# Kernel tuning notes

Measured on AMD Instinct MI355X. Metric: run time of the kernel, lower is better.

## Reference

```python
import jax, jax.numpy as jnp
import numpy as np

D = 512      # d_model
H = 8        # num_heads
DH = D // H  # d_head = 64
WIN = 10     # window_size
DFF = 2048   # d_ff
EPS = 1e-5   # LayerNorm eps


def _layernorm(x, w, b):
    mu = jnp.mean(x, axis=-1, keepdims=True)
    var = jnp.mean(jnp.square(x - mu), axis=-1, keepdims=True)
    return (x - mu) * jax.lax.rsqrt(var + EPS) * w + b


def setup_inputs() -> dict:
    key = jax.random.key(0)
    ks = jax.random.split(key, 8)
    s = 0.02
    inp = {
        "z": jax.random.normal(ks[0], (4, 2048, D), jnp.float32),
        "Wq": jax.random.normal(ks[1], (D, D), jnp.float32) * s,
        "bq": jnp.zeros((D,), jnp.float32),
        "Wk": jax.random.normal(ks[2], (D, D), jnp.float32) * s,
        "bk": jnp.zeros((D,), jnp.float32),
        "Wv": jax.random.normal(ks[3], (D, D), jnp.float32) * s,
        "bv": jnp.zeros((D,), jnp.float32),
        "Wo": jax.random.normal(ks[4], (D, D), jnp.float32) * s,
        "bo": jnp.zeros((D,), jnp.float32),
        "ln1_w": jnp.ones((D,), jnp.float32),
        "ln1_b": jnp.zeros((D,), jnp.float32),
        "W1": jax.random.normal(ks[5], (D, DFF), jnp.float32) * s,
        "b1": jnp.zeros((DFF,), jnp.float32),
        "W2": jax.random.normal(ks[6], (DFF, D), jnp.float32) * s,
        "b2": jnp.zeros((D,), jnp.float32),
        "ln2_w": jnp.ones((D,), jnp.float32),
        "ln2_b": jnp.zeros((D,), jnp.float32),
    }
    return inp


def reference(z, Wq, bq, Wk, bk, Wv, bv, Wo, bo, ln1_w, ln1_b, W1, b1, W2, b2, ln2_w, ln2_b):
    B, T, Dm = z.shape
    # projections -> [B, H, T, DH]
    q = (z @ Wq + bq).reshape(B, T, H, DH).transpose(0, 2, 1, 3)
    k = (z @ Wk + bk).reshape(B, T, H, DH).transpose(0, 2, 1, 3)
    v = (z @ Wv + bv).reshape(B, T, H, DH).transpose(0, 2, 1, 3)
    scale = 1.0 / jnp.sqrt(jnp.asarray(DH, z.dtype))
    scores = jnp.einsum('bhqd,bhkd->bhqk', q, k) * scale  # [B,H,T,T]
    idx = jnp.arange(T)
    dist = idx[:, None] - idx[None, :]
    valid = (dist >= 0) & (dist < WIN)
    neg = jnp.finfo(scores.dtype).min
    scores = jnp.where(valid[None, None], scores, neg)
    attn = jax.nn.softmax(scores, axis=-1)  # dropout is identity in eval
    out = jnp.einsum('bhqk,bhkd->bhqd', attn, v)
    out = out.transpose(0, 2, 1, 3).reshape(B, T, Dm)
    out = out @ Wo + bo
    z = _layernorm(z + out, ln1_w, ln1_b)
    # FFN with exact (erf) GELU, matching torch nn.GELU default
    ff = jax.nn.gelu(z @ W1 + b1, approximate=False) @ W2 + b2
    z = _layernorm(z + ff, ln2_w, ln2_b)
    return z
```

## Files before the change

### kernel.cpp

```cpp
#include <hip/hip_runtime.h>
#include <cstdint>
#include <cstddef>

#define DEV __device__ __forceinline__

typedef __bf16 bf16x8 __attribute__((ext_vector_type(8)));
typedef float f32x4 __attribute__((ext_vector_type(4)));
typedef unsigned short us8 __attribute__((ext_vector_type(8)));
typedef unsigned short us4 __attribute__((ext_vector_type(4)));

typedef const __attribute__((address_space(1))) unsigned int GUI;
typedef __attribute__((address_space(3))) unsigned int LUI;

DEV unsigned short f2bf(float f) {
  unsigned int u = __builtin_bit_cast(unsigned int, f);
  u += 0x7fffu + ((u >> 16) & 1u);
  return (unsigned short)(u >> 16);
}
DEV float bf2f(unsigned short h) {
  unsigned int u = ((unsigned int)h) << 16;
  return __builtin_bit_cast(float, u);
}

DEV void tr32(const float* __restrict__ in, unsigned short* __restrict__ out,
              int K, int N, int k0, int n0) {
  __shared__ float tile[32][33];
  const int tx = threadIdx.x & 31, ty = threadIdx.x >> 5;
#pragma unroll
  for (int i = 0; i < 32; i += 8)
    tile[ty + i][tx] = in[(size_t)(k0 + ty + i) * N + n0 + tx];
  __syncthreads();
#pragma unroll
  for (int i = 0; i < 32; i += 8)
    out[(size_t)(n0 + ty + i) * K + k0 + tx] = f2bf(tile[tx][ty + i]);
}

__global__ __launch_bounds__(256) void k_prep(
    const float* __restrict__ z, unsigned short* __restrict__ zb,
    const float* __restrict__ Wq, const float* __restrict__ Wk,
    const float* __restrict__ Wv, const float* __restrict__ Wo,
    unsigned short* __restrict__ Wsq,
    const float* __restrict__ W1, unsigned short* __restrict__ W1T,
    const float* __restrict__ W2, unsigned short* __restrict__ W2T,
    const float* __restrict__ bq, const float* __restrict__ bk,
    const float* __restrict__ bv, float* __restrict__ biasqkv) {
  const int j = blockIdx.x;
  const int tid = threadIdx.x;
  if (j < 4096) {
    int i = j * 256 + tid;
    float4 v = ((const float4*)z)[i];
    us4 o;
    o.x = f2bf(v.x); o.y = f2bf(v.y); o.z = f2bf(v.z); o.w = f2bf(v.w);
    *(us4*)(zb + (size_t)i * 4) = o;
  } else if (j < 5120) {
    int t = j - 4096;
    int mat = t >> 8, tile = t & 255;
    const float* in = mat == 0 ? Wq : mat == 1 ? Wk : mat == 2 ? Wv : Wo;
    tr32(in, Wsq + (size_t)mat * 262144, 512, 512, (tile >> 4) * 32, (tile & 15) * 32);
  } else if (j < 6144) {
    int t = j - 5120;
    tr32(W1, W1T, 512, 2048, (t / 64) * 32, (t % 64) * 32);
  } else if (j < 7168) {
    int t = j - 6144;
    tr32(W2, W2T, 2048, 512, (t / 16) * 32, (t % 16) * 32);
  } else {
    for (int i = tid; i < 1536; i += 256)
      biasqkv[i] = (i < 512) ? bq[i] : (i < 1024 ? bk[i - 512] : bv[i - 1024]);
  }
}

template <int MODE, int SPLITK>
DEV void gemm_body(const unsigned short* __restrict__ A,
                   const unsigned short* __restrict__ BT,
                   const float* __restrict__ bias,
                   unsigned short* __restrict__ outp,
                   int K, int N) {
  __shared__ __align__(16) unsigned short As[2 * 16384];
  __shared__ __align__(16) unsigned short Bs[2 * 16384];
  const int tid = threadIdx.x;
  const int wave = tid >> 6, lane = tid & 63;
  const int wm = wave >> 2, wn = wave & 3;

  const int nx = gridDim.x, ny = gridDim.y;
  const int nwg = nx * ny * SPLITK;
  const int lid = (blockIdx.z * ny + blockIdx.y) * nx + blockIdx.x;
  const int q8 = nwg >> 3, r8 = nwg & 7;
  const int xcd = lid & 7, slot = lid >> 3;
  const int wid = (xcd < r8 ? xcd * (q8 + 1) : r8 * (q8 + 1) + (xcd - r8) * q8) + slot;
  const int nbz = nx * SPLITK;
  const int bxz = wid % nbz;
  const int by  = wid / nbz;
  const int bx  = bxz % nx;
  const int z   = bxz / nx;

  const int rbase = by * 256;
  const int nbase = bx * 256;
  const int nkt = (K / SPLITK) >> 6;
  const int kb = z * (K / SPLITK);

  float bv_[4];
#pragma unroll
  for (int n = 0; n < 4; ++n) {
    int gcol = nbase + wn * 64 + n * 16 + (lane & 15);
    bv_[n] = (z == 0) ? bias[gcol] : 0.f;
  }
  asm volatile("s_waitcnt vmcnt(0)" ::: "memory");

  auto STAGE = [&](int buf, int k0) {
#pragma unroll
    for (int t = 0; t < 4; ++t) {
      int s = t * 512 + tid;
      int row = s >> 3;
      int col = ((s & 7) ^ (row & 7)) << 3;
      const unsigned short* ga = A + (size_t)(rbase + row) * K + k0 + col;
      const unsigned short* gb = BT + (size_t)(nbase + row) * K + k0 + col;
      const int dst = buf * 16384 + (t * 512 + wave * 64) * 8;
      __builtin_amdgcn_global_load_lds((GUI*)ga, (LUI*)(As + dst), 16, 0, 0);
      __builtin_amdgcn_global_load_lds((GUI*)gb, (LUI*)(Bs + dst), 16, 0, 0);
    }
  };

  f32x4 acc[8][4] = {};
  STAGE(0, kb);

  for (int kt = 0; kt < nkt; ++kt) {
    const int cur = kt & 1;
    if (kt + 1 < nkt) {
      STAGE(cur ^ 1, kb + (kt + 1) * 64);
      asm volatile("s_waitcnt vmcnt(8)" ::: "memory");
    } else {
      asm volatile("s_waitcnt vmcnt(0)" ::: "memory");
    }
    __builtin_amdgcn_s_barrier();

#pragma unroll
    for (int ks = 0; ks < 2; ++ks) {
      bf16x8 af[8], bfr[4];
#pragma unroll
      for (int m = 0; m < 8; ++m) {
        int row = wm * 128 + m * 16 + (lane & 15);
        int ch = (ks * 4 + (lane >> 4)) ^ (row & 7);
        af[m] = __builtin_bit_cast(bf16x8, *(const us8*)(As + cur * 16384 + row * 64 + ch * 8));
      }
#pragma unroll
      for (int n = 0; n < 4; ++n) {
        int row = wn * 64 + n * 16 + (lane & 15);
        int ch = (ks * 4 + (lane >> 4)) ^ (row & 7);
        bfr[n] = __builtin_bit_cast(bf16x8, *(const us8*)(Bs + cur * 16384 + row * 64 + ch * 8));
      }
      __builtin_amdgcn_s_setprio(1);
#pragma unroll
      for (int m = 0; m < 8; ++m)
#pragma unroll
        for (int n = 0; n < 4; ++n)
          acc[m][n] = __builtin_amdgcn_mfma_f32_16x16x32_bf16(af[m], bfr[n], acc[m][n], 0, 0, 0);
      __builtin_amdgcn_s_setprio(0);
    }
    asm volatile("s_waitcnt lgkmcnt(0)" ::: "memory");
    __builtin_amdgcn_s_barrier();
  }

  unsigned short* opv = outp + (size_t)z * 8192 * N;
#pragma unroll
  for (int m = 0; m < 8; ++m) {
    int grow0 = rbase + wm * 128 + m * 16 + ((lane >> 4) << 2);
#pragma unroll
    for (int n = 0; n < 4; ++n) {
      int gcol = nbase + wn * 64 + n * 16 + (lane & 15);
#pragma unroll
      for (int r = 0; r < 4; ++r) {
        float v = acc[m][n][r] + bv_[n];
        if (MODE == 2) v = 0.5f * v * (1.0f + erff(v * 0.70710678118654752f));
        opv[(size_t)(grow0 + r) * N + gcol] = f2bf(v);
      }
    }
  }
}

__global__ __launch_bounds__(512) void k_qkv(const unsigned short* __restrict__ A,
                                             const unsigned short* __restrict__ BT,
                                             const float* __restrict__ bias,
                                             unsigned short* __restrict__ outp, int K, int N) {
  gemm_body<0, 1>(A, BT, bias, outp, K, N);
}
__global__ __launch_bounds__(512) void k_wo(const unsigned short* __restrict__ A,
                                            const unsigned short* __restrict__ BT,
                                            const float* __restrict__ bias,
                                            unsigned short* __restrict__ outp, int K, int N) {
  gemm_body<0, 4>(A, BT, bias, outp, K, N);
}
__global__ __launch_bounds__(512) void k_ffn1(const unsigned short* __restrict__ A,
                                              const unsigned short* __restrict__ BT,
                                              const float* __restrict__ bias,
                                              unsigned short* __restrict__ outp, int K, int N) {
  gemm_body<2, 1>(A, BT, bias, outp, K, N);
}
__global__ __launch_bounds__(512) void k_ffn2(const unsigned short* __restrict__ A,
                                              const unsigned short* __restrict__ BT,
                                              const float* __restrict__ bias,
                                              unsigned short* __restrict__ outp, int K, int N) {
  gemm_body<0, 4>(A, BT, bias, outp, K, N);
}

__global__ __launch_bounds__(64) void k_attn(const unsigned short* __restrict__ qkv,
                                             unsigned short* __restrict__ attnb) {
  __shared__ float Qt[64 * 67];
  __shared__ float Kt[64 * 75];
  __shared__ float P[64 * 12];

  const int lane = threadIdx.x;
  const int bid = blockIdx.x;
  const int chunk = bid & 31;
  const int bh = bid >> 5;
  const int h = bh & 7, b = bh >> 3;
  const int i0 = chunk * 64;
  const int b2048 = b * 2048;
  const int h64 = h * 64;

#pragma unroll 8
  for (int r = 0; r < 73; ++r) {
    int jloc = i0 - 9 + r;
    int jc = jloc < 0 ? 0 : jloc;
    Kt[lane * 75 + r] = bf2f(qkv[(size_t)(b2048 + jc) * 1536 + 512 + h64 + lane]);
  }
#pragma unroll 8
  for (int r = 0; r < 64; ++r) {
    Qt[lane * 67 + r] = bf2f(qkv[(size_t)(b2048 + i0 + r) * 1536 + h64 + lane]);
  }
  __syncthreads();

  float s[10];
#pragma unroll
  for (int jj = 0; jj < 10; ++jj) s[jj] = 0.f;
#pragma unroll
  for (int d = 0; d < 64; ++d) {
    float qd = Qt[d * 67 + lane];
#pragma unroll
    for (int jj = 0; jj < 10; ++jj)
      s[jj] = fmaf(qd, Kt[d * 75 + lane + jj], s[jj]);
  }
  const int iG = i0 + lane;
#pragma unroll
  for (int jj = 0; jj < 10; ++jj)
    s[jj] = (iG - 9 + jj >= 0) ? s[jj] * 0.125f : -1e30f;
  float mx = s[9];
#pragma unroll
  for (int jj = 0; jj < 9; ++jj) mx = fmaxf(mx, s[jj]);
  float den = 0.f;
#pragma unroll
  for (int jj = 0; jj < 10; ++jj) {
    s[jj] = __expf(s[jj] - mx);
    den += s[jj];
  }
  float inv = 1.f / den;
#pragma unroll
  for (int jj = 0; jj < 10; ++jj) P[lane * 12 + jj] = s[jj] * inv;
  __syncthreads();

  for (int q0 = 0; q0 < 64; q0 += 4) {
    float vv[13];
#pragma unroll
    for (int t = 0; t < 13; ++t) {
      int jloc = i0 + q0 - 9 + t;
      int jc = jloc < 0 ? 0 : jloc;
      vv[t] = bf2f(qkv[(size_t)(b2048 + jc) * 1536 + 1024 + h64 + lane]);
    }
#pragma unroll
    for (int qq = 0; qq < 4; ++qq) {
      const int q = q0 + qq;
      const float* pp = &P[q * 12];
      float o = 0.f;
#pragma unroll
      for (int jj = 0; jj < 10; ++jj) o = fmaf(pp[jj], vv[qq + jj], o);
      attnb[(size_t)(b2048 + i0 + q) * 512 + h64 + lane] = f2bf(o);
    }
  }
}

template <int OUTF32, int NP>
DEV void ln_body(const unsigned short* __restrict__ res,
                 const unsigned short* __restrict__ add,
                 const float* __restrict__ w,
                 const float* __restrict__ bb,
                 void* __restrict__ outp) {
  const size_t PLANE = (size_t)8192 * 512;
  const int wave = threadIdx.x >> 6, lane = threadIdx.x & 63;
  const int row = blockIdx.x * 4 + wave;
  float x[8];
  us8 r = *(const us8*)(res + (size_t)row * 512 + lane * 8);
#pragma unroll
  for (int j = 0; j < 8; ++j) x[j] = bf2f(r[j]);
#pragma unroll
  for (int p = 0; p < NP; ++p) {
    us8 a = *(const us8*)(add + p * PLANE + (size_t)row * 512 + lane * 8);
#pragma unroll
    for (int j = 0; j < 8; ++j) x[j] += bf2f(a[j]);
  }
  float sum = 0.f, ss = 0.f;
#pragma unroll
  for (int j = 0; j < 8; ++j) {
    sum += x[j];
    ss += x[j] * x[j];
  }
#pragma unroll
  for (int m = 32; m >= 1; m >>= 1) {
    sum += __shfl_xor(sum, m);
    ss += __shfl_xor(ss, m);
  }
  const float mu = sum * (1.f / 512.f);
  float var = ss * (1.f / 512.f) - mu * mu;
  const float rstd = rsqrtf(var + 1e-5f);
  const int c = lane * 8;
  float o[8];
#pragma unroll
  for (int j = 0; j < 8; ++j) o[j] = (x[j] - mu) * rstd * w[c + j] + bb[c + j];
  if (OUTF32 == 0) {
    us8 u;
#pragma unroll
    for (int j = 0; j < 8; ++j) u[j] = f2bf(o[j]);
    *(us8*)((unsigned short*)outp + (size_t)row * 512 + c) = u;
  } else {
    float4 u0, u1;
    u0.x = o[0]; u0.y = o[1]; u0.z = o[2]; u0.w = o[3];
    u1.x = o[4]; u1.y = o[5]; u1.z = o[6]; u1.w = o[7];
    float4* o4 = (float4*)((float*)outp + (size_t)row * 512 + c);
    o4[0] = u0; o4[1] = u1;
  }
}

__global__ __launch_bounds__(256) void k_ln_mid(const unsigned short* __restrict__ res,
                                                const unsigned short* __restrict__ add,
                                                const float* __restrict__ w,
                                                const float* __restrict__ bb,
                                                unsigned short* __restrict__ outp) {
  ln_body<0, 4>(res, add, w, bb, outp);
}
__global__ __launch_bounds__(256) void k_ln_out(const unsigned short* __restrict__ res,
                                                const unsigned short* __restrict__ add,
                                                const float* __restrict__ w,
                                                const float* __restrict__ bb,
                                                float* __restrict__ outp) {
  ln_body<1, 4>(res, add, w, bb, outp);
}

extern "C" void kernel_launch(void* const* d_in, const int* in_sizes, int n_in,
                              void* d_out, int out_size, void* d_ws, size_t ws_size,
                              hipStream_t stream) {
  const float* z    = (const float*)d_in[0];
  const float* Wq   = (const float*)d_in[1];
  const float* bq   = (const float*)d_in[2];
  const float* Wk   = (const float*)d_in[3];
  const float* bk   = (const float*)d_in[4];
  const float* Wv   = (const float*)d_in[5];
  const float* bv   = (const float*)d_in[6];
  const float* Wo   = (const float*)d_in[7];
  const float* bo   = (const float*)d_in[8];
  const float* ln1w = (const float*)d_in[9];
  const float* ln1b = (const float*)d_in[10];
  const float* W1   = (const float*)d_in[11];
  const float* b1   = (const float*)d_in[12];
  const float* W2   = (const float*)d_in[13];
  const float* b2   = (const float*)d_in[14];
  const float* ln2w = (const float*)d_in[15];
  const float* ln2b = (const float*)d_in[16];
  float* out = (float*)d_out;

  char* ws = (char*)d_ws;
  size_t off = 0;
  auto alloc = [&](size_t bytes) {
    char* p = ws + off;
    off += (bytes + 255) & ~(size_t)255;
    return p;
  };
  unsigned short* Wsq   = (unsigned short*)alloc((size_t)2048 * 512 * 2);
  unsigned short* WTqkv = Wsq;
  unsigned short* WoT   = Wsq + (size_t)1536 * 512;
  unsigned short* W1T   = (unsigned short*)alloc((size_t)2048 * 512 * 2);
  unsigned short* W2T   = (unsigned short*)alloc((size_t)512 * 2048 * 2);
  float*          biasqkv = (float*)alloc(1536 * 4);
  unsigned short* zb    = (unsigned short*)alloc((size_t)8192 * 512 * 2);
  unsigned short* z1b   = (unsigned short*)alloc((size_t)8192 * 512 * 2);
  unsigned short* qkvb  = (unsigned short*)alloc((size_t)8192 * 1536 * 2);
  unsigned short* attnb = (unsigned short*)alloc((size_t)8192 * 512 * 2);
  unsigned short* p1    = (unsigned short*)alloc((size_t)4 * 8192 * 512 * 2);
  unsigned short* ff    = qkvb;

  k_prep<<<7169, 256, 0, stream>>>(z, zb, Wq, Wk, Wv, Wo, Wsq, W1, W1T, W2, W2T,
                                   bq, bk, bv, biasqkv);
  k_qkv<<<dim3(6, 32), 512, 0, stream>>>(zb, WTqkv, biasqkv, qkvb, 512, 1536);
  k_attn<<<1024, 64, 0, stream>>>(qkvb, attnb);
  k_wo<<<dim3(2, 32, 4), 512, 0, stream>>>(attnb, WoT, bo, p1, 512, 512);
  k_ln_mid<<<2048, 256, 0, stream>>>(zb, p1, ln1w, ln1b, z1b);
  k_ffn1<<<dim3(8, 32), 512, 0, stream>>>(z1b, W1T, b1, ff, 512, 2048);
  k_ffn2<<<dim3(2, 32, 4), 512, 0, stream>>>(ff, W2T, b2, p1, 2048, 512);
  k_ln_out<<<2048, 256, 0, stream>>>(z1b, p1, ln2w, ln2b, out);
}
```

Measured before the change: 143.6 us.

## Split GEMM K-tile into four barrier-separated phases and halve attention query chunks

```diff
diff --git a/kernel.cpp b/kernel.cpp
--- a/kernel.cpp
+++ b/kernel.cpp
@@ -80,6 +80,7 @@
   const int tid = threadIdx.x;
   const int wave = tid >> 6, lane = tid & 63;
   const int wm = wave >> 2, wn = wave & 3;
+  const int q = lane >> 4, l15 = lane & 15;
 
   const int nx = gridDim.x, ny = gridDim.y;
   const int nwg = nx * ny * SPLITK;
@@ -101,14 +102,14 @@
   float bv_[4];
 #pragma unroll
   for (int n = 0; n < 4; ++n) {
-    int gcol = nbase + wn * 64 + n * 16 + (lane & 15);
+    int gcol = nbase + wn * 64 + n * 16 + l15;
     bv_[n] = (z == 0) ? bias[gcol] : 0.f;
   }
   asm volatile("s_waitcnt vmcnt(0)" ::: "memory");
 
-  auto STAGE = [&](int buf, int k0) {
-#pragma unroll
-    for (int t = 0; t < 4; ++t) {
+  auto STAGE2 = [&](int buf, int k0, int t0) {
+#pragma unroll
+    for (int t = t0; t < t0 + 2; ++t) {
       int s = t * 512 + tid;
       int row = s >> 3;
       int col = ((s & 7) ^ (row & 7)) << 3;
@@ -120,53 +121,91 @@
     }
   };
 
+  auto LDA = [&](const unsigned short* Ab, int ks, int mh, bf16x8* af) {
+#pragma unroll
+    for (int m = 0; m < 4; ++m) {
+      int row = wm * 128 + (mh * 4 + m) * 16 + l15;
+      int ch = (ks * 4 + q) ^ (row & 7);
+      af[m] = __builtin_bit_cast(bf16x8, *(const us8*)(Ab + row * 64 + ch * 8));
+    }
+  };
+  auto LDB = [&](const unsigned short* Bb, int ks, bf16x8* bfr) {
+#pragma unroll
+    for (int n = 0; n < 4; ++n) {
+      int row = wn * 64 + n * 16 + l15;
+      int ch = (ks * 4 + q) ^ (row & 7);
+      bfr[n] = __builtin_bit_cast(bf16x8, *(const us8*)(Bb + row * 64 + ch * 8));
+    }
+  };
+
   f32x4 acc[8][4] = {};
-  STAGE(0, kb);
-
-  for (int kt = 0; kt < nkt; ++kt) {
-    const int cur = kt & 1;
-    if (kt + 1 < nkt) {
-      STAGE(cur ^ 1, kb + (kt + 1) * 64);
-      asm volatile("s_waitcnt vmcnt(8)" ::: "memory");
-    } else {
-      asm volatile("s_waitcnt vmcnt(0)" ::: "memory");
-    }
-    __builtin_amdgcn_s_barrier();
-
-#pragma unroll
-    for (int ks = 0; ks < 2; ++ks) {
-      bf16x8 af[8], bfr[4];
-#pragma unroll
-      for (int m = 0; m < 8; ++m) {
-        int row = wm * 128 + m * 16 + (lane & 15);
-        int ch = (ks * 4 + (lane >> 4)) ^ (row & 7);
-        af[m] = __builtin_bit_cast(bf16x8, *(const us8*)(As + cur * 16384 + row * 64 + ch * 8));
-      }
-#pragma unroll
-      for (int n = 0; n < 4; ++n) {
-        int row = wn * 64 + n * 16 + (lane & 15);
-        int ch = (ks * 4 + (lane >> 4)) ^ (row & 7);
-        bfr[n] = __builtin_bit_cast(bf16x8, *(const us8*)(Bs + cur * 16384 + row * 64 + ch * 8));
-      }
-      __builtin_amdgcn_s_setprio(1);
-#pragma unroll
-      for (int m = 0; m < 8; ++m)
-#pragma unroll
-        for (int n = 0; n < 4; ++n)
-          acc[m][n] = __builtin_amdgcn_mfma_f32_16x16x32_bf16(af[m], bfr[n], acc[m][n], 0, 0, 0);
-      __builtin_amdgcn_s_setprio(0);
-    }
-    asm volatile("s_waitcnt lgkmcnt(0)" ::: "memory");
-    __builtin_amdgcn_s_barrier();
-  }
+  bf16x8 af[4], bfr0[4], bfr1[4];
+
+  STAGE2(0, kb, 0);
+  STAGE2(0, kb, 2);
+  asm volatile("s_waitcnt vmcnt(0)" ::: "memory");
+  __builtin_amdgcn_s_barrier();
+
+#define PHASE_TAIL                                     \
+  asm volatile("s_waitcnt lgkmcnt(0)" ::: "memory");   \
+  __builtin_amdgcn_sched_barrier(0);                   \
+  __builtin_amdgcn_s_setprio(1);
+
+#define MFMA16(AF, BF, MH)                                                        \
+  _Pragma("unroll") for (int m = 0; m < 4; ++m)                                   \
+  _Pragma("unroll") for (int n = 0; n < 4; ++n)                                   \
+    acc[MH * 4 + m][n] = __builtin_amdgcn_mfma_f32_16x16x32_bf16(AF[m], BF[n], acc[MH * 4 + m][n], 0, 0, 0);
+
+  for (int t = 0; t < nkt; ++t) {
+    const int cur = t & 1;
+    const unsigned short* Ab = As + cur * 16384;
+    const unsigned short* Bb = Bs + cur * 16384;
+    const bool pre = (t + 1 < nkt);
+    const int knext = kb + (t + 1) * 64;
+
+    LDA(Ab, 0, 0, af);
+    LDB(Bb, 0, bfr0);
+    if (pre) STAGE2(cur ^ 1, knext, 0);
+    __builtin_amdgcn_s_barrier();
+    PHASE_TAIL
+    MFMA16(af, bfr0, 0)
+    __builtin_amdgcn_s_setprio(0);
+    __builtin_amdgcn_s_barrier();
+
+    LDA(Ab, 1, 0, af);
+    LDB(Bb, 1, bfr1);
+    if (pre) STAGE2(cur ^ 1, knext, 2);
+    __builtin_amdgcn_s_barrier();
+    PHASE_TAIL
+    MFMA16(af, bfr1, 0)
+    __builtin_amdgcn_s_setprio(0);
+    __builtin_amdgcn_s_barrier();
+
+    LDA(Ab, 0, 1, af);
+    __builtin_amdgcn_s_barrier();
+    PHASE_TAIL
+    MFMA16(af, bfr0, 1)
+    __builtin_amdgcn_s_setprio(0);
+    __builtin_amdgcn_s_barrier();
+
+    LDA(Ab, 1, 1, af);
+    if (pre) asm volatile("s_waitcnt vmcnt(0)" ::: "memory");
+    __builtin_amdgcn_s_barrier();
+    PHASE_TAIL
+    MFMA16(af, bfr1, 1)
+    __builtin_amdgcn_s_setprio(0);
+    __builtin_amdgcn_s_barrier();
+  }
+#undef PHASE_TAIL
+#undef MFMA16
 
   unsigned short* opv = outp + (size_t)z * 8192 * N;
 #pragma unroll
   for (int m = 0; m < 8; ++m) {
-    int grow0 = rbase + wm * 128 + m * 16 + ((lane >> 4) << 2);
+    int grow0 = rbase + wm * 128 + m * 16 + (q << 2);
 #pragma unroll
     for (int n = 0; n < 4; ++n) {
-      int gcol = nbase + wn * 64 + n * 16 + (lane & 15);
+      int gcol = nbase + wn * 64 + n * 16 + l15;
 #pragma unroll
       for (int r = 0; r < 4; ++r) {
         float v = acc[m][n][r] + bv_[n];
@@ -204,42 +243,47 @@
 
 __global__ __launch_bounds__(64) void k_attn(const unsigned short* __restrict__ qkv,
                                              unsigned short* __restrict__ attnb) {
-  __shared__ float Qt[64 * 67];
-  __shared__ float Kt[64 * 75];
-  __shared__ float P[64 * 12];
+  __shared__ float Qt[64 * 35];
+  __shared__ float Kt[64 * 45];
+  __shared__ float P[32 * 12];
 
   const int lane = threadIdx.x;
   const int bid = blockIdx.x;
-  const int chunk = bid & 31;
-  const int bh = bid >> 5;
+  const int chunk = bid & 63;
+  const int bh = bid >> 6;
   const int h = bh & 7, b = bh >> 3;
-  const int i0 = chunk * 64;
+  const int i0 = chunk * 32;
   const int b2048 = b * 2048;
   const int h64 = h * 64;
 
 #pragma unroll 8
-  for (int r = 0; r < 73; ++r) {
+  for (int r = 0; r < 41; ++r) {
     int jloc = i0 - 9 + r;
     int jc = jloc < 0 ? 0 : jloc;
-    Kt[lane * 75 + r] = bf2f(qkv[(size_t)(b2048 + jc) * 1536 + 512 + h64 + lane]);
+    Kt[lane * 45 + r] = bf2f(qkv[(size_t)(b2048 + jc) * 1536 + 512 + h64 + lane]);
   }
 #pragma unroll 8
-  for (int r = 0; r < 64; ++r) {
-    Qt[lane * 67 + r] = bf2f(qkv[(size_t)(b2048 + i0 + r) * 1536 + h64 + lane]);
+  for (int r = 0; r < 32; ++r) {
+    Qt[lane * 35 + r] = bf2f(qkv[(size_t)(b2048 + i0 + r) * 1536 + h64 + lane]);
   }
   __syncthreads();
 
+  const int qe = lane & 31, dh = lane >> 5;
   float s[10];
 #pragma unroll
   for (int jj = 0; jj < 10; ++jj) s[jj] = 0.f;
 #pragma unroll
-  for (int d = 0; d < 64; ++d) {
-    float qd = Qt[d * 67 + lane];
+  for (int dd = 0; dd < 32; ++dd) {
+    int d = dh * 32 + dd;
+    float qd = Qt[d * 35 + qe];
 #pragma unroll
     for (int jj = 0; jj < 10; ++jj)
-      s[jj] = fmaf(qd, Kt[d * 75 + lane + jj], s[jj]);
-  }
-  const int iG = i0 + lane;
+      s[jj] = fmaf(qd, Kt[d * 45 + qe + jj], s[jj]);
+  }
+#pragma unroll
+  for (int jj = 0; jj < 10; ++jj) s[jj] += __shfl_xor(s[jj], 32);
+
+  const int iG = i0 + qe;
 #pragma unroll
   for (int jj = 0; jj < 10; ++jj)
     s[jj] = (iG - 9 + jj >= 0) ? s[jj] * 0.125f : -1e30f;
@@ -253,11 +297,13 @@
     den += s[jj];
   }
   float inv = 1.f / den;
-#pragma unroll
-  for (int jj = 0; jj < 10; ++jj) P[lane * 12 + jj] = s[jj] * inv;
+  if (lane < 32) {
+#pragma unroll
+    for (int jj = 0; jj < 10; ++jj) P[qe * 12 + jj] = s[jj] * inv;
+  }
   __syncthreads();
 
-  for (int q0 = 0; q0 < 64; q0 += 4) {
+  for (int q0 = 0; q0 < 32; q0 += 4) {
     float vv[13];
 #pragma unroll
     for (int t = 0; t < 13; ++t) {
@@ -267,12 +313,12 @@
     }
 #pragma unroll
     for (int qq = 0; qq < 4; ++qq) {
-      const int q = q0 + qq;
-      const float* pp = &P[q * 12];
+      const int qy = q0 + qq;
+      const float* pp = &P[qy * 12];
       float o = 0.f;
 #pragma unroll
       for (int jj = 0; jj < 10; ++jj) o = fmaf(pp[jj], vv[qq + jj], o);
-      attnb[(size_t)(b2048 + i0 + q) * 512 + h64 + lane] = f2bf(o);
+      attnb[(size_t)(b2048 + i0 + qy) * 512 + h64 + lane] = f2bf(o);
     }
   }
 }
@@ -388,7 +434,7 @@
   k_prep<<<7169, 256, 0, stream>>>(z, zb, Wq, Wk, Wv, Wo, Wsq, W1, W1T, W2, W2T,
                                    bq, bk, bv, biasqkv);
   k_qkv<<<dim3(6, 32), 512, 0, stream>>>(zb, WTqkv, biasqkv, qkvb, 512, 1536);
-  k_attn<<<1024, 64, 0, stream>>>(qkvb, attnb);
+  k_attn<<<2048, 64, 0, stream>>>(qkvb, attnb);
   k_wo<<<dim3(2, 32, 4), 512, 0, stream>>>(attnb, WoT, bo, p1, 512, 512);
   k_ln_mid<<<2048, 256, 0, stream>>>(zb, p1, ln1w, ln1b, z1b);
   k_ffn1<<<dim3(8, 32), 512, 0, stream>>>(z1b, W1T, b1, ff, 512, 2048);
```

After: 145.0 us. No clear change (+1.0%).

## Fuse local attention, output projection and first LayerNorm into one kernel

Applied to the files above, without the earlier changes.

```diff
diff --git a/kernel.cpp b/kernel.cpp
--- a/kernel.cpp
+++ b/kernel.cpp
@@ -70,11 +70,11 @@
 }
 
 template <int MODE, int SPLITK>
-DEV void gemm_body(const unsigned short* __restrict__ A,
-                   const unsigned short* __restrict__ BT,
-                   const float* __restrict__ bias,
-                   unsigned short* __restrict__ outp,
-                   int K, int N) {
+DEV void gemm256_body(const unsigned short* __restrict__ A,
+                      const unsigned short* __restrict__ BT,
+                      const float* __restrict__ bias,
+                      unsigned short* __restrict__ outp,
+                      int K, int N) {
   __shared__ __align__(16) unsigned short As[2 * 16384];
   __shared__ __align__(16) unsigned short Bs[2 * 16384];
   const int tid = threadIdx.x;
@@ -181,65 +181,75 @@
                                              const unsigned short* __restrict__ BT,
                                              const float* __restrict__ bias,
                                              unsigned short* __restrict__ outp, int K, int N) {
-  gemm_body<0, 1>(A, BT, bias, outp, K, N);
-}
-__global__ __launch_bounds__(512) void k_wo(const unsigned short* __restrict__ A,
-                                            const unsigned short* __restrict__ BT,
-                                            const float* __restrict__ bias,
-                                            unsigned short* __restrict__ outp, int K, int N) {
-  gemm_body<0, 4>(A, BT, bias, outp, K, N);
+  gemm256_body<0, 1>(A, BT, bias, outp, K, N);
 }
 __global__ __launch_bounds__(512) void k_ffn1(const unsigned short* __restrict__ A,
                                               const unsigned short* __restrict__ BT,
                                               const float* __restrict__ bias,
                                               unsigned short* __restrict__ outp, int K, int N) {
-  gemm_body<2, 1>(A, BT, bias, outp, K, N);
+  gemm256_body<2, 1>(A, BT, bias, outp, K, N);
 }
 __global__ __launch_bounds__(512) void k_ffn2(const unsigned short* __restrict__ A,
                                               const unsigned short* __restrict__ BT,
                                               const float* __restrict__ bias,
                                               unsigned short* __restrict__ outp, int K, int N) {
-  gemm_body<0, 4>(A, BT, bias, outp, K, N);
-}
-
-__global__ __launch_bounds__(64) void k_attn(const unsigned short* __restrict__ qkv,
-                                             unsigned short* __restrict__ attnb) {
-  __shared__ float Qt[64 * 67];
-  __shared__ float Kt[64 * 75];
-  __shared__ float P[64 * 12];
-
-  const int lane = threadIdx.x;
+  gemm256_body<0, 4>(A, BT, bias, outp, K, N);
+}
+
+__global__ __launch_bounds__(512) void k_awl(
+    const unsigned short* __restrict__ qkv,
+    const unsigned short* __restrict__ WoT,
+    const float* __restrict__ bo,
+    const unsigned short* __restrict__ zb,
+    const float* __restrict__ ln1w, const float* __restrict__ ln1b,
+    unsigned short* __restrict__ z1b) {
+  __shared__ __align__(16) char smem[137728];
+  unsigned short* aout = (unsigned short*)smem;
+  float* Kt = (float*)(smem + 33280);
+  float* P  = (float*)(smem + 125440);
+  unsigned short* Bst = (unsigned short*)(smem + 33280);
+  float* part = (float*)(smem + 98816);
+  float* lnp  = (float*)(smem + 100864);
+
+  const int tid = threadIdx.x;
+  const int w = tid >> 6, lane = tid & 63;
   const int bid = blockIdx.x;
-  const int chunk = bid & 31;
-  const int bh = bid >> 5;
-  const int h = bh & 7, b = bh >> 3;
-  const int i0 = chunk * 64;
+  const int b = bid >> 6;
+  const int i0 = (bid & 63) * 32;
   const int b2048 = b * 2048;
-  const int h64 = h * 64;
-
+  const int h64 = w * 64;
+
+  float* KtH = Kt + w * (64 * 45);
 #pragma unroll 8
-  for (int r = 0; r < 73; ++r) {
+  for (int r = 0; r < 41; ++r) {
     int jloc = i0 - 9 + r;
     int jc = jloc < 0 ? 0 : jloc;
-    Kt[lane * 75 + r] = bf2f(qkv[(size_t)(b2048 + jc) * 1536 + 512 + h64 + lane]);
-  }
-#pragma unroll 8
-  for (int r = 0; r < 64; ++r) {
-    Qt[lane * 67 + r] = bf2f(qkv[(size_t)(b2048 + i0 + r) * 1536 + h64 + lane]);
-  }
-  __syncthreads();
-
+    KtH[lane * 45 + r] = bf2f(qkv[(size_t)(b2048 + jc) * 1536 + 512 + h64 + lane]);
+  }
+  const int qe = lane & 31, dh = lane >> 5;
+  us8 qreg[4];
+  {
+    const unsigned short* qp = qkv + (size_t)(b2048 + i0 + qe) * 1536 + h64 + dh * 32;
+#pragma unroll
+    for (int t = 0; t < 4; ++t) qreg[t] = *(const us8*)(qp + t * 8);
+  }
   float s[10];
 #pragma unroll
   for (int jj = 0; jj < 10; ++jj) s[jj] = 0.f;
 #pragma unroll
-  for (int d = 0; d < 64; ++d) {
-    float qd = Qt[d * 67 + lane];
-#pragma unroll
-    for (int jj = 0; jj < 10; ++jj)
-      s[jj] = fmaf(qd, Kt[d * 75 + lane + jj], s[jj]);
-  }
-  const int iG = i0 + lane;
+  for (int t = 0; t < 4; ++t) {
+#pragma unroll
+    for (int e = 0; e < 8; ++e) {
+      float qd = bf2f(qreg[t][e]);
+      int d = dh * 32 + t * 8 + e;
+#pragma unroll
+      for (int jj = 0; jj < 10; ++jj)
+        s[jj] = fmaf(qd, KtH[d * 45 + qe + jj], s[jj]);
+    }
+  }
+#pragma unroll
+  for (int jj = 0; jj < 10; ++jj) s[jj] += __shfl_xor(s[jj], 32);
+  const int iG = i0 + qe;
 #pragma unroll
   for (int jj = 0; jj < 10; ++jj)
     s[jj] = (iG - 9 + jj >= 0) ? s[jj] * 0.125f : -1e30f;
@@ -253,11 +263,11 @@
     den += s[jj];
   }
   float inv = 1.f / den;
-#pragma unroll
-  for (int jj = 0; jj < 10; ++jj) P[lane * 12 + jj] = s[jj] * inv;
-  __syncthreads();
-
-  for (int q0 = 0; q0 < 64; q0 += 4) {
+  if (lane < 32) {
+#pragma unroll
+    for (int jj = 0; jj < 10; ++jj) P[(w * 32 + qe) * 12 + jj] = s[jj] * inv;
+  }
+  for (int q0 = 0; q0 < 32; q0 += 4) {
     float vv[13];
 #pragma unroll
     for (int t = 0; t < 13; ++t) {
@@ -267,22 +277,140 @@
     }
 #pragma unroll
     for (int qq = 0; qq < 4; ++qq) {
-      const int q = q0 + qq;
-      const float* pp = &P[q * 12];
+      const int qy = q0 + qq;
+      const float* pp = &P[(w * 32 + qy) * 12];
       float o = 0.f;
 #pragma unroll
       for (int jj = 0; jj < 10; ++jj) o = fmaf(pp[jj], vv[qq + jj], o);
-      attnb[(size_t)(b2048 + i0 + q) * 512 + h64 + lane] = f2bf(o);
-    }
-  }
-}
-
-template <int OUTF32, int NP>
-DEV void ln_body(const unsigned short* __restrict__ res,
-                 const unsigned short* __restrict__ add,
-                 const float* __restrict__ w,
-                 const float* __restrict__ bb,
-                 void* __restrict__ outp) {
+      aout[qy * 520 + h64 + lane] = f2bf(o);
+    }
+  }
+  __syncthreads();
+
+  const int q4 = lane >> 4, l15 = lane & 15;
+  auto STAGE = [&](int buf, int k0) {
+#pragma unroll
+    for (int t = 0; t < 4; ++t) {
+      int sI = t * 512 + tid;
+      int R = sI >> 3;
+      int c = (sI & 7) ^ (R & 7);
+      int rr = 2 * R + (c >> 2);
+      int kl = (c & 3) << 3;
+      const unsigned short* gb = WoT + (size_t)rr * 512 + k0 + kl;
+      const int dst = buf * 16384 + (t * 512 + w * 64) * 8;
+      __builtin_amdgcn_global_load_lds((GUI*)gb, (LUI*)(Bst + dst), 16, 0, 0);
+    }
+  };
+  asm volatile("s_waitcnt vmcnt(0)" ::: "memory");
+  STAGE(0, 0);
+  f32x4 acc[2][4] = {};
+  for (int kt = 0; kt < 16; ++kt) {
+    const int cur = kt & 1;
+    if (kt + 1 < 16) {
+      STAGE(cur ^ 1, (kt + 1) * 32);
+      asm volatile("s_waitcnt vmcnt(4)" ::: "memory");
+    } else {
+      asm volatile("s_waitcnt vmcnt(0)" ::: "memory");
+    }
+    __builtin_amdgcn_s_barrier();
+    bf16x8 af[2], bfr[4];
+#pragma unroll
+    for (int m = 0; m < 2; ++m) {
+      int row = m * 16 + l15;
+      af[m] = __builtin_bit_cast(bf16x8, *(const us8*)(aout + row * 520 + kt * 32 + q4 * 8));
+    }
+#pragma unroll
+    for (int n = 0; n < 4; ++n) {
+      int rr = h64 + n * 16 + l15;
+      int R = rr >> 1;
+      int d = (((rr & 1) << 2) + q4) ^ (R & 7);
+      bfr[n] = __builtin_bit_cast(bf16x8, *(const us8*)(Bst + cur * 16384 + R * 64 + d * 8));
+    }
+    asm volatile("s_waitcnt lgkmcnt(0)" ::: "memory");
+    __builtin_amdgcn_sched_barrier(0);
+    __builtin_amdgcn_s_setprio(1);
+#pragma unroll
+    for (int m = 0; m < 2; ++m)
+#pragma unroll
+      for (int n = 0; n < 4; ++n)
+        acc[m][n] = __builtin_amdgcn_mfma_f32_16x16x32_bf16(af[m], bfr[n], acc[m][n], 0, 0, 0);
+    __builtin_amdgcn_s_setprio(0);
+    __builtin_amdgcn_s_barrier();
+  }
+
+  float x[2][4][4];
+  float psum[8], pss[8];
+#pragma unroll
+  for (int m = 0; m < 8; ++m) { psum[m] = 0.f; pss[m] = 0.f; }
+#pragma unroll
+  for (int m = 0; m < 2; ++m) {
+#pragma unroll
+    for (int n = 0; n < 4; ++n) {
+      int col = h64 + n * 16 + l15;
+      float bv = bo[col];
+#pragma unroll
+      for (int r = 0; r < 4; ++r) {
+        int row = m * 16 + (q4 << 2) + r;
+        float v = acc[m][n][r] + bv + bf2f(zb[(size_t)(b2048 + i0 + row) * 512 + col]);
+        x[m][n][r] = v;
+        psum[m * 4 + r] += v;
+        pss[m * 4 + r] += v * v;
+      }
+    }
+  }
+#pragma unroll
+  for (int m = 0; m < 8; ++m) {
+#pragma unroll
+    for (int o = 1; o < 16; o <<= 1) {
+      psum[m] += __shfl_xor(psum[m], o);
+      pss[m]  += __shfl_xor(pss[m], o);
+    }
+  }
+  if (l15 == 0) {
+#pragma unroll
+    for (int m = 0; m < 2; ++m)
+#pragma unroll
+      for (int r = 0; r < 4; ++r) {
+        int row = m * 16 + (q4 << 2) + r;
+        part[(row * 8 + w) * 2 + 0] = psum[m * 4 + r];
+        part[(row * 8 + w) * 2 + 1] = pss[m * 4 + r];
+      }
+  }
+  __syncthreads();
+  if (w == 0 && lane < 32) {
+    float su = 0.f, ssq = 0.f;
+#pragma unroll
+    for (int p = 0; p < 8; ++p) {
+      su  += part[(lane * 8 + p) * 2 + 0];
+      ssq += part[(lane * 8 + p) * 2 + 1];
+    }
+    float mu = su * (1.f / 512.f);
+    float var = ssq * (1.f / 512.f) - mu * mu;
+    lnp[lane * 2 + 0] = mu;
+    lnp[lane * 2 + 1] = rsqrtf(var + 1e-5f);
+  }
+  __syncthreads();
+#pragma unroll
+  for (int m = 0; m < 2; ++m) {
+#pragma unroll
+    for (int n = 0; n < 4; ++n) {
+      int col = h64 + n * 16 + l15;
+      float wv = ln1w[col], bbv = ln1b[col];
+#pragma unroll
+      for (int r = 0; r < 4; ++r) {
+        int row = m * 16 + (q4 << 2) + r;
+        float o = (x[m][n][r] - lnp[row * 2]) * lnp[row * 2 + 1] * wv + bbv;
+        z1b[(size_t)(b2048 + i0 + row) * 512 + col] = f2bf(o);
+      }
+    }
+  }
+}
+
+__global__ __launch_bounds__(256) void k_ln_out(const unsigned short* __restrict__ res,
+                                                const unsigned short* __restrict__ add,
+                                                const float* __restrict__ w,
+                                                const float* __restrict__ bb,
+                                                float* __restrict__ outp) {
   const size_t PLANE = (size_t)8192 * 512;
   const int wave = threadIdx.x >> 6, lane = threadIdx.x & 63;
   const int row = blockIdx.x * 4 + wave;
@@ -291,7 +419,7 @@
 #pragma unroll
   for (int j = 0; j < 8; ++j) x[j] = bf2f(r[j]);
 #pragma unroll
-  for (int p = 0; p < NP; ++p) {
+  for (int p = 0; p < 4; ++p) {
     us8 a = *(const us8*)(add + p * PLANE + (size_t)row * 512 + lane * 8);
 #pragma unroll
     for (int j = 0; j < 8; ++j) x[j] += bf2f(a[j]);
@@ -311,36 +439,14 @@
   float var = ss * (1.f / 512.f) - mu * mu;
   const float rstd = rsqrtf(var + 1e-5f);
   const int c = lane * 8;
+  float4 u0, u1;
   float o[8];
 #pragma unroll
   for (int j = 0; j < 8; ++j) o[j] = (x[j] - mu) * rstd * w[c + j] + bb[c + j];
-  if (OUTF32 == 0) {
-    us8 u;
-#pragma unroll
-    for (int j = 0; j < 8; ++j) u[j] = f2bf(o[j]);
-    *(us8*)((unsigned short*)outp + (size_t)row * 512 + c) = u;
-  } else {
-    float4 u0, u1;
-    u0.x = o[0]; u0.y = o[1]; u0.z = o[2]; u0.w = o[3];
-    u1.x = o[4]; u1.y = o[5]; u1.z = o[6]; u1.w = o[7];
-    float4* o4 = (float4*)((float*)outp + (size_t)row * 512 + c);
-    o4[0] = u0; o4[1] = u1;
-  }
-}
-
-__global__ __launch_bounds__(256) void k_ln_mid(const unsigned short* __restrict__ res,
-                                                const unsigned short* __restrict__ add,
-                                                const float* __restrict__ w,
-                                                const float* __restrict__ bb,
-                                                unsigned short* __restrict__ outp) {
-  ln_body<0, 4>(res, add, w, bb, outp);
-}
-__global__ __launch_bounds__(256) void k_ln_out(const unsigned short* __restrict__ res,
-                                                const unsigned short* __restrict__ add,
-                                                const float* __restrict__ w,
-                                                const float* __restrict__ bb,
-                                                float* __restrict__ outp) {
-  ln_body<1, 4>(res, add, w, bb, outp);
+  u0.x = o[0]; u0.y = o[1]; u0.z = o[2]; u0.w = o[3];
+  u1.x = o[4]; u1.y = o[5]; u1.z = o[6]; u1.w = o[7];
+  float4* o4 = (float4*)(outp + (size_t)row * 512 + c);
+  o4[0] = u0; o4[1] = u1;
 }
 
 extern "C" void kernel_launch(void* const* d_in, const int* in_sizes, int n_in,
@@ -381,16 +487,13 @@
   unsigned short* zb    = (unsigned short*)alloc((size_t)8192 * 512 * 2);
   unsigned short* z1b   = (unsigned short*)alloc((size_t)8192 * 512 * 2);
   unsigned short* qkvb  = (unsigned short*)alloc((size_t)8192 * 1536 * 2);
-  unsigned short* attnb = (unsigned short*)alloc((size_t)8192 * 512 * 2);
   unsigned short* p1    = (unsigned short*)alloc((size_t)4 * 8192 * 512 * 2);
   unsigned short* ff    = qkvb;
 
   k_prep<<<7169, 256, 0, stream>>>(z, zb, Wq, Wk, Wv, Wo, Wsq, W1, W1T, W2, W2T,
                                    bq, bk, bv, biasqkv);
   k_qkv<<<dim3(6, 32), 512, 0, stream>>>(zb, WTqkv, biasqkv, qkvb, 512, 1536);
-  k_attn<<<1024, 64, 0, stream>>>(qkvb, attnb);
-  k_wo<<<dim3(2, 32, 4), 512, 0, stream>>>(attnb, WoT, bo, p1, 512, 512);
-  k_ln_mid<<<2048, 256, 0, stream>>>(zb, p1, ln1w, ln1b, z1b);
+  k_awl<<<256, 512, 0, stream>>>(qkvb, WoT, bo, zb, ln1w, ln1b, z1b);
   k_ffn1<<<dim3(8, 32), 512, 0, stream>>>(z1b, W1T, b1, ff, 512, 2048);
   k_ffn2<<<dim3(2, 32, 4), 512, 0, stream>>>(ff, W2T, b2, p1, 2048, 512);
   k_ln_out<<<2048, 256, 0, stream>>>(z1b, p1, ln2w, ln2b, out);
```

Result: faster. 128.9 us (-10.2%).
